# Optimization experiments

Measured on AMD Instinct MI355X. Metric: run time of the kernel, lower is better.

## Reference

```python
import jax, jax.numpy as jnp
import numpy as np
from jax import lax

T = 5        # unrolled ISTA iterations (module default)
LAM = 0.1    # soft-threshold level (module default)
B, L, K = 4096, 4096, 128


def _conv1d_same(x, k):
    """TF-style SAME cross-correlation. x: [B, L], k: [K] -> [B, L]."""
    Kw = k.shape[0]
    pad_left = (Kw - 1) // 2
    pad_right = Kw - 1 - pad_left
    out = lax.conv_general_dilated(
        x[:, None, :],            # [B, 1, L]
        k[None, None, :],         # [O=1, I=1, K]
        window_strides=(1,),
        padding=[(pad_left, pad_right)],
        dimension_numbers=("NCH", "OIH", "NCH"),
    )
    return out[:, 0, :]


def setup_inputs() -> dict:
    key = jax.random.key(0)
    k1, k2 = jax.random.split(key)
    y = jax.random.normal(k1, (B, L), dtype=jnp.float32)
    thz_pulse = jax.random.normal(k2, (K,), dtype=jnp.float32)  # learned pulse (trainable)
    step_size = jnp.full((1,), 0.1, dtype=jnp.float32)          # learned step (trainable)
    return {"y": y, "thz_pulse": thz_pulse, "step_size": step_size}


def reference(y, thz_pulse, step_size):
    x = jnp.zeros_like(y)
    h = thz_pulse           # matched-filter kernel
    h_rev = thz_pulse[::-1] # time-reversed kernel (adjoint / correlation)
    s = step_size[0]
    for _ in range(T):
        conv_out = _conv1d_same(y, h)           # H y
        residual = y - conv_out                 # y - H y
        update = _conv1d_same(residual, h_rev)  # H^T residual
        x = x + s * update                      # gradient step
        x = jnp.sign(x) * jax.nn.relu(jnp.abs(x) - LAM)  # soft-threshold
    return x
```

## Files before the change

### kernel.cpp

```cpp
#include <hip/hip_runtime.h>


typedef __bf16 bf16;
typedef __bf16 bf16x4 __attribute__((ext_vector_type(4)));
typedef __bf16 bf16x8 __attribute__((ext_vector_type(8)));
typedef float f32x4 __attribute__((ext_vector_type(4)));

#define LC 512
#define PY 824
#define LAM 0.1f
#define WS_AG 0
#define WS_A1 8192
#define WS_A2 12288
#define PYE 360
#define PRE 216

__global__ __launch_bounds__(256) void ista_prep(const float* __restrict__ h,
                                                 bf16* __restrict__ ws) {
  __shared__ float hs[256];
  __shared__ float acp[256];
  __shared__ bf16 gp[384];
  const int tid = threadIdx.x;
  hs[tid] = (tid < 128) ? h[tid] : 0.f;
  gp[tid] = (bf16)0.f;
  if (tid < 128) gp[256 + tid] = (bf16)0.f;
  __syncthreads();
  const int tau = tid & 127;
  {
    const int m0 = (tid >> 7) * 64;
    float p0 = 0.f, p1 = 0.f, p2 = 0.f, p3 = 0.f;
    for (int m = m0; m < m0 + 64; m += 4) {
      p0 += hs[m] * hs[m + tau];     p1 += hs[m + 1] * hs[m + 1 + tau];
      p2 += hs[m + 2] * hs[m + 2 + tau]; p3 += hs[m + 3] * hs[m + 3 + tau];
    }
    acp[tid] = (p0 + p1) + (p2 + p3);
  }
  __syncthreads();
  if (tid < 128) {
    float ac = acp[tid] + acp[tid + 128];
    float g1 = (tau <= 63) ? hs[63 - tau] : 0.f;
    gp[145 + tau] = (bf16)(g1 - ac);
    if (tau > 0) {
      float g2 = (tau <= 64) ? hs[63 + tau] : 0.f;
      gp[145 - tau] = (bf16)(g2 - ac);
    }
  }
  __syncthreads();
  for (int i = tid; i < 1024; i += 256) {
    const int l = i >> 4, dd = i & 15;
    if (dd < 9) {
      const int o = 144 + (l >> 4) * 8 - (l & 15) + (dd - 4) * 32;
      bf16x8 a;
#pragma unroll
      for (int j = 0; j < 8; ++j) a[j] = gp[o + j];
      *reinterpret_cast<bf16x8*>(ws + WS_AG + l * 128 + dd * 8) = a;
    }
  }
  for (int i = tid; i < 512; i += 256) {
    const int l = i >> 3, dd = i & 7;
    if (dd < 5) {
      const int o = 127 + (l >> 4) * 8 - (l & 15) + (dd - 2) * 32;
      bf16x8 a1, a2;
#pragma unroll
      for (int j = 0; j < 8; ++j) {
        int p = o + j;
        int i1 = p - 64;
        a1[j] = ((unsigned)i1 < 128u) ? (bf16)hs[i1] : (bf16)0.f;
        int i2 = 191 - p;
        a2[j] = ((unsigned)i2 < 128u) ? (bf16)(-hs[i2]) : (bf16)0.f;
      }
      *reinterpret_cast<bf16x8*>(ws + WS_A1 + l * 64 + dd * 8) = a1;
      *reinterpret_cast<bf16x8*>(ws + WS_A2 + l * 64 + dd * 8) = a2;
    }
  }
}

__global__ __launch_bounds__(256) void ista_fused(
    const float* __restrict__ y, const bf16* __restrict__ ws,
    const float* __restrict__ step, float* __restrict__ out) {
  __shared__ __align__(16) bf16 buf[16 * PY];
  const int tid = threadIdx.x;
  const int lane = tid & 63;
  const int li = lane & 15;
  const int quad = lane >> 4;
  const int wave = tid >> 6;
  const int bid = blockIdx.x;
  const float s = step[0];

  if (bid < 2048) {
    const int chunk0 = (bid >> 8) * LC;
    const int b0 = (bid & 255) * 16;

    bf16x8 AG[9];
#pragma unroll
    for (int dd = 0; dd < 9; ++dd)
      AG[dd] = *reinterpret_cast<const bf16x8*>(ws + WS_AG + lane * 128 + dd * 8);

    {
      const int rr = tid >> 4;
      const int t = tid & 15;
      const float* yrow = y + (size_t)(b0 + rr) * 4096;
      bf16* dst = buf + rr * PY;
      if (chunk0 != 0 && chunk0 != 3584) {
#pragma unroll
        for (int k = 0; k < 13; ++k) {
          int s4 = t + 16 * k;
          if (s4 < 200) {
            float4 v = *reinterpret_cast<const float4*>(yrow + chunk0 - 128 + s4 * 4);
            bf16x4 bv;
            bv[0] = (bf16)v.x; bv[1] = (bf16)v.y; bv[2] = (bf16)v.z; bv[3] = (bf16)v.w;
            *reinterpret_cast<bf16x4*>(dst + s4 * 4) = bv;
          }
        }
      } else {
#pragma unroll
        for (int k = 0; k < 13; ++k) {
          int s4 = t + 16 * k;
          if (s4 < 200) {
            int l = chunk0 - 128 + s4 * 4;
            float4 v;
            if (l >= 0 && l <= 4096 - 4) {
              v = *reinterpret_cast<const float4*>(yrow + l);
            } else {
              v.x = ((unsigned)(l + 0) < 4096u) ? yrow[l + 0] : 0.f;
              v.y = ((unsigned)(l + 1) < 4096u) ? yrow[l + 1] : 0.f;
              v.z = ((unsigned)(l + 2) < 4096u) ? yrow[l + 2] : 0.f;
              v.w = ((unsigned)(l + 3) < 4096u) ? yrow[l + 3] : 0.f;
            }
            bf16x4 bv;
            bv[0] = (bf16)v.x; bv[1] = (bf16)v.y; bv[2] = (bf16)v.z; bv[3] = (bf16)v.w;
            *reinterpret_cast<bf16x4*>(dst + s4 * 4) = bv;
          }
        }
      }
    }
    __syncthreads();

    const bf16* brow = buf + li * PY + 128 + quad * 8;
    const int iw = 16 * wave;
    bf16x8 B[9];
#pragma unroll
    for (int dd = 0; dd < 9; ++dd)
      B[dd] = *reinterpret_cast<const bf16x8*>(brow + iw + (dd - 4) * 32);
    float* orow = out + (size_t)(b0 + li) * 4096 + chunk0 + iw + quad * 4;
#pragma unroll
    for (int k = 0; k < 8; ++k) {
      f32x4 acc0 = {0.f, 0.f, 0.f, 0.f};
      f32x4 acc1 = {0.f, 0.f, 0.f, 0.f};
      acc0 = __builtin_amdgcn_mfma_f32_16x16x32_bf16(AG[0], B[0], acc0, 0, 0, 0);
      acc1 = __builtin_amdgcn_mfma_f32_16x16x32_bf16(AG[1], B[1], acc1, 0, 0, 0);
      acc0 = __builtin_amdgcn_mfma_f32_16x16x32_bf16(AG[2], B[2], acc0, 0, 0, 0);
      acc1 = __builtin_amdgcn_mfma_f32_16x16x32_bf16(AG[3], B[3], acc1, 0, 0, 0);
      acc0 = __builtin_amdgcn_mfma_f32_16x16x32_bf16(AG[4], B[4], acc0, 0, 0, 0);
      acc1 = __builtin_amdgcn_mfma_f32_16x16x32_bf16(AG[5], B[5], acc1, 0, 0, 0);
      acc0 = __builtin_amdgcn_mfma_f32_16x16x32_bf16(AG[6], B[6], acc0, 0, 0, 0);
      acc1 = __builtin_amdgcn_mfma_f32_16x16x32_bf16(AG[7], B[7], acc1, 0, 0, 0);
      acc0 = __builtin_amdgcn_mfma_f32_16x16x32_bf16(AG[8], B[8], acc0, 0, 0, 0);
      const int gc0 = chunk0 + iw + 64 * k;
      if (gc0 >= 64 && gc0 < 4032) {
        float4 xv;
#pragma unroll
        for (int e = 0; e < 4; ++e) {
          float su = s * (acc0[e] + acc1[e]);
          float ax = fabsf(su) - LAM;
          ax = ax > 0.f ? ax : 0.f;
          (&xv.x)[e] = 5.f * copysignf(ax, su);
        }
        *reinterpret_cast<float4*>(orow + 64 * k) = xv;
      }
      if (k < 7) {
#pragma unroll
        for (int r = 0; r < 7; ++r) B[r] = B[r + 2];
        B[7] = *reinterpret_cast<const bf16x8*>(brow + iw + 64 * (k + 1) + 96);
        B[8] = *reinterpret_cast<const bf16x8*>(brow + iw + 64 * (k + 1) + 128);
      }
    }
  } else {
    const int eid = bid - 2048;
    const int chunk0 = (eid & 1) ? (4096 - 64) : 0;
    const int b0 = (eid >> 1) * 16;
    bf16* ys = buf;
    bf16* rs = buf + 16 * PYE;

    bf16x8 A1[5], A2[5];
#pragma unroll
    for (int dd = 0; dd < 5; ++dd) {
      A1[dd] = *reinterpret_cast<const bf16x8*>(ws + WS_A1 + lane * 64 + dd * 8);
      A2[dd] = *reinterpret_cast<const bf16x8*>(ws + WS_A2 + lane * 64 + dd * 8);
    }

    {
      const int rr = tid >> 4;
      const int t = tid & 15;
      const float* yrow = y + (size_t)(b0 + rr) * 4096;
      bf16* dst = ys + rr * PYE;
#pragma unroll
      for (int k = 0; k < 6; ++k) {
        int s4 = t + 16 * k;
        if (s4 < 88) {
          int l = chunk0 - 128 + s4 * 4;
          float4 v;
          if (l >= 0 && l <= 4096 - 4) {
            v = *reinterpret_cast<const float4*>(yrow + l);
          } else {
            v.x = ((unsigned)(l + 0) < 4096u) ? yrow[l + 0] : 0.f;
            v.y = ((unsigned)(l + 1) < 4096u) ? yrow[l + 1] : 0.f;
            v.z = ((unsigned)(l + 2) < 4096u) ? yrow[l + 2] : 0.f;
            v.w = ((unsigned)(l + 3) < 4096u) ? yrow[l + 3] : 0.f;
          }
          bf16x4 bv;
          bv[0] = (bf16)v.x; bv[1] = (bf16)v.y; bv[2] = (bf16)v.z; bv[3] = (bf16)v.w;
          *reinterpret_cast<bf16x4*>(dst + s4 * 4) = bv;
        }
      }
    }
    __syncthreads();

    for (int t = wave; t < 13; t += 4) {
      const int i0 = -64 + 16 * t;
      f32x4 acc;
      {
        bf16x4 yv = *reinterpret_cast<const bf16x4*>(
            ys + li * PYE + (i0 + 128) + quad * 4);
        acc[0] = -(float)yv[0]; acc[1] = -(float)yv[1];
        acc[2] = -(float)yv[2]; acc[3] = -(float)yv[3];
      }
#pragma unroll
      for (int dd = 0; dd < 5; ++dd) {
        bf16x8 b = *reinterpret_cast<const bf16x8*>(
            ys + li * PYE + (i0 + (dd - 2) * 32 + 128) + quad * 8);
        acc = __builtin_amdgcn_mfma_f32_16x16x32_bf16(A1[dd], b, acc, 0, 0, 0);
      }
      bf16x4 rv;
#pragma unroll
      for (int e = 0; e < 4; ++e) {
        int g = chunk0 + i0 + quad * 4 + e;
        float v = ((unsigned)g < 4096u) ? acc[e] : 0.f;
        rv[e] = (bf16)v;
      }
      *reinterpret_cast<bf16x4*>(rs + li * PRE + (i0 + 64) + quad * 4) = rv;
    }
    __syncthreads();

    {
      const int i0 = 16 * wave;
      f32x4 acc = {0.f, 0.f, 0.f, 0.f};
#pragma unroll
      for (int dd = 0; dd < 5; ++dd) {
        bf16x8 b = *reinterpret_cast<const bf16x8*>(
            rs + li * PRE + (i0 + (dd - 2) * 32 + 64) + quad * 8);
        acc = __builtin_amdgcn_mfma_f32_16x16x32_bf16(A2[dd], b, acc, 0, 0, 0);
      }
      float4 xv;
#pragma unroll
      for (int e = 0; e < 4; ++e) {
        float su = s * acc[e];
        float ax = fabsf(su) - LAM;
        ax = ax > 0.f ? ax : 0.f;
        (&xv.x)[e] = 5.f * copysignf(ax, su);
      }
      *reinterpret_cast<float4*>(
          out + (size_t)(b0 + li) * 4096 + chunk0 + i0 + quad * 4) = xv;
    }
  }
}

extern "C" void kernel_launch(void* const* d_in, const int* in_sizes, int n_in,
                              void* d_out, int out_size, void* d_ws,
                              size_t ws_size, hipStream_t stream) {
  const float* y = (const float*)d_in[0];
  const float* h = (const float*)d_in[1];
  const float* s = (const float*)d_in[2];
  float* out = (float*)d_out;
  bf16* ws = (bf16*)d_ws;
  ista_prep<<<dim3(1), dim3(256), 0, stream>>>(h, ws);
  ista_fused<<<dim3(2048 + 512), dim3(256), 0, stream>>>(y, ws, s, out);
}
```

Measured before the change: 133.1 us.

## Load interior conv windows directly from global memory, dropping LDS staging

The interior path no longer stages a bf16 copy of the y tile in shared memory behind a block barrier. Each lane now loads its own 8-element windows straight from global memory, converts them to bf16 in registers, and prefetches the next two windows ahead of the MFMA chain. The shared buffer shrinks to what the edge path needs, and launch bounds now request 4 blocks per CU. The cost is redundant global loads, since neighbouring windows overlap and are fetched several times through the cache instead of once.

```diff
diff --git a/kernel.cpp b/kernel.cpp
--- a/kernel.cpp
+++ b/kernel.cpp
@@ -7,7 +7,6 @@
 typedef float f32x4 __attribute__((ext_vector_type(4)));
 
 #define LC 512
-#define PY 824
 #define LAM 0.1f
 #define WS_AG 0
 #define WS_A1 8192
@@ -75,10 +74,95 @@
   }
 }
 
-__global__ __launch_bounds__(256) void ista_fused(
+template <bool SAFE>
+__device__ __forceinline__ bf16x8 load_win(const float* __restrict__ yrow,
+                                           int c) {
+  bf16x8 b;
+  if (SAFE || (c >= 0 && c <= 4096 - 8)) {
+    float4 v0 = *reinterpret_cast<const float4*>(yrow + c);
+    float4 v1 = *reinterpret_cast<const float4*>(yrow + c + 4);
+    b[0] = (bf16)v0.x; b[1] = (bf16)v0.y; b[2] = (bf16)v0.z; b[3] = (bf16)v0.w;
+    b[4] = (bf16)v1.x; b[5] = (bf16)v1.y; b[6] = (bf16)v1.z; b[7] = (bf16)v1.w;
+  } else {
+#pragma unroll
+    for (int j = 0; j < 8; ++j) {
+      int cc = c + j;
+      b[j] = ((unsigned)cc < 4096u) ? (bf16)yrow[cc] : (bf16)0.f;
+    }
+  }
+  return b;
+}
+
+template <bool SAFE>
+__device__ __forceinline__ void interior_path(
+    const float* __restrict__ y, const bf16* __restrict__ ws, float s,
+    float* __restrict__ out, int chunk0, int b0, int lane) {
+  const int li = lane & 15;
+  const int quad = lane >> 4;
+  const int wave = (threadIdx.x) >> 6;
+
+  bf16x8 AG[9];
+#pragma unroll
+  for (int dd = 0; dd < 9; ++dd)
+    AG[dd] = *reinterpret_cast<const bf16x8*>(ws + WS_AG + lane * 128 + dd * 8);
+
+  const float* yrow = y + (size_t)(b0 + li) * 4096;
+  const int iw = 16 * wave;
+  const int cb = chunk0 + iw + quad * 8;
+
+  bf16x8 B[9];
+#pragma unroll
+  for (int dd = 0; dd < 9; ++dd)
+    B[dd] = load_win<SAFE>(yrow, cb + (dd - 4) * 32);
+
+  float* orow = out + (size_t)(b0 + li) * 4096 + chunk0 + iw + quad * 4;
+#pragma unroll
+  for (int k = 0; k < 8; ++k) {
+    bf16x8 n0, n1;
+    if (k < 7) {
+      n0 = load_win<SAFE>(yrow, cb + 64 * (k + 1) + 96);
+      n1 = load_win<SAFE>(yrow, cb + 64 * (k + 1) + 128);
+    }
+    f32x4 acc0 = {0.f, 0.f, 0.f, 0.f};
+    f32x4 acc1 = {0.f, 0.f, 0.f, 0.f};
+    acc0 = __builtin_amdgcn_mfma_f32_16x16x32_bf16(AG[0], B[0], acc0, 0, 0, 0);
+    acc1 = __builtin_amdgcn_mfma_f32_16x16x32_bf16(AG[1], B[1], acc1, 0, 0, 0);
+    acc0 = __builtin_amdgcn_mfma_f32_16x16x32_bf16(AG[2], B[2], acc0, 0, 0, 0);
+    acc1 = __builtin_amdgcn_mfma_f32_16x16x32_bf16(AG[3], B[3], acc1, 0, 0, 0);
+    acc0 = __builtin_amdgcn_mfma_f32_16x16x32_bf16(AG[4], B[4], acc0, 0, 0, 0);
+    acc1 = __builtin_amdgcn_mfma_f32_16x16x32_bf16(AG[5], B[5], acc1, 0, 0, 0);
+    acc0 = __builtin_amdgcn_mfma_f32_16x16x32_bf16(AG[6], B[6], acc0, 0, 0, 0);
+    acc1 = __builtin_amdgcn_mfma_f32_16x16x32_bf16(AG[7], B[7], acc1, 0, 0, 0);
+    acc0 = __builtin_amdgcn_mfma_f32_16x16x32_bf16(AG[8], B[8], acc0, 0, 0, 0);
+    bool do_store = true;
+    if (!SAFE) {
+      const int gc0 = chunk0 + iw + 64 * k;
+      do_store = (gc0 >= 64 && gc0 < 4032);
+    }
+    if (do_store) {
+      float4 xv;
+#pragma unroll
+      for (int e = 0; e < 4; ++e) {
+        float su = s * (acc0[e] + acc1[e]);
+        float ax = fabsf(su) - LAM;
+        ax = ax > 0.f ? ax : 0.f;
+        (&xv.x)[e] = 5.f * copysignf(ax, su);
+      }
+      *reinterpret_cast<float4*>(orow + 64 * k) = xv;
+    }
+    if (k < 7) {
+#pragma unroll
+      for (int r = 0; r < 7; ++r) B[r] = B[r + 2];
+      B[7] = n0;
+      B[8] = n1;
+    }
+  }
+}
+
+__global__ __launch_bounds__(256, 4) void ista_fused(
     const float* __restrict__ y, const bf16* __restrict__ ws,
     const float* __restrict__ step, float* __restrict__ out) {
-  __shared__ __align__(16) bf16 buf[16 * PY];
+  __shared__ __align__(16) bf16 buf[16 * PYE + 16 * PRE];
   const int tid = threadIdx.x;
   const int lane = tid & 63;
   const int li = lane & 15;
@@ -90,90 +174,10 @@
   if (bid < 2048) {
     const int chunk0 = (bid >> 8) * LC;
     const int b0 = (bid & 255) * 16;
-
-    bf16x8 AG[9];
-#pragma unroll
-    for (int dd = 0; dd < 9; ++dd)
-      AG[dd] = *reinterpret_cast<const bf16x8*>(ws + WS_AG + lane * 128 + dd * 8);
-
-    {
-      const int rr = tid >> 4;
-      const int t = tid & 15;
-      const float* yrow = y + (size_t)(b0 + rr) * 4096;
-      bf16* dst = buf + rr * PY;
-      if (chunk0 != 0 && chunk0 != 3584) {
-#pragma unroll
-        for (int k = 0; k < 13; ++k) {
-          int s4 = t + 16 * k;
-          if (s4 < 200) {
-            float4 v = *reinterpret_cast<const float4*>(yrow + chunk0 - 128 + s4 * 4);
-            bf16x4 bv;
-            bv[0] = (bf16)v.x; bv[1] = (bf16)v.y; bv[2] = (bf16)v.z; bv[3] = (bf16)v.w;
-            *reinterpret_cast<bf16x4*>(dst + s4 * 4) = bv;
-          }
-        }
-      } else {
-#pragma unroll
-        for (int k = 0; k < 13; ++k) {
-          int s4 = t + 16 * k;
-          if (s4 < 200) {
-            int l = chunk0 - 128 + s4 * 4;
-            float4 v;
-            if (l >= 0 && l <= 4096 - 4) {
-              v = *reinterpret_cast<const float4*>(yrow + l);
-            } else {
-              v.x = ((unsigned)(l + 0) < 4096u) ? yrow[l + 0] : 0.f;
-              v.y = ((unsigned)(l + 1) < 4096u) ? yrow[l + 1] : 0.f;
-              v.z = ((unsigned)(l + 2) < 4096u) ? yrow[l + 2] : 0.f;
-              v.w = ((unsigned)(l + 3) < 4096u) ? yrow[l + 3] : 0.f;
-            }
-            bf16x4 bv;
-            bv[0] = (bf16)v.x; bv[1] = (bf16)v.y; bv[2] = (bf16)v.z; bv[3] = (bf16)v.w;
-            *reinterpret_cast<bf16x4*>(dst + s4 * 4) = bv;
-          }
-        }
-      }
-    }
-    __syncthreads();
-
-    const bf16* brow = buf + li * PY + 128 + quad * 8;
-    const int iw = 16 * wave;
-    bf16x8 B[9];
-#pragma unroll
-    for (int dd = 0; dd < 9; ++dd)
-      B[dd] = *reinterpret_cast<const bf16x8*>(brow + iw + (dd - 4) * 32);
-    float* orow = out + (size_t)(b0 + li) * 4096 + chunk0 + iw + quad * 4;
-#pragma unroll
-    for (int k = 0; k < 8; ++k) {
-      f32x4 acc0 = {0.f, 0.f, 0.f, 0.f};
-      f32x4 acc1 = {0.f, 0.f, 0.f, 0.f};
-      acc0 = __builtin_amdgcn_mfma_f32_16x16x32_bf16(AG[0], B[0], acc0, 0, 0, 0);
-      acc1 = __builtin_amdgcn_mfma_f32_16x16x32_bf16(AG[1], B[1], acc1, 0, 0, 0);
-      acc0 = __builtin_amdgcn_mfma_f32_16x16x32_bf16(AG[2], B[2], acc0, 0, 0, 0);
-      acc1 = __builtin_amdgcn_mfma_f32_16x16x32_bf16(AG[3], B[3], acc1, 0, 0, 0);
-      acc0 = __builtin_amdgcn_mfma_f32_16x16x32_bf16(AG[4], B[4], acc0, 0, 0, 0);
-      acc1 = __builtin_amdgcn_mfma_f32_16x16x32_bf16(AG[5], B[5], acc1, 0, 0, 0);
-      acc0 = __builtin_amdgcn_mfma_f32_16x16x32_bf16(AG[6], B[6], acc0, 0, 0, 0);
-      acc1 = __builtin_amdgcn_mfma_f32_16x16x32_bf16(AG[7], B[7], acc1, 0, 0, 0);
-      acc0 = __builtin_amdgcn_mfma_f32_16x16x32_bf16(AG[8], B[8], acc0, 0, 0, 0);
-      const int gc0 = chunk0 + iw + 64 * k;
-      if (gc0 >= 64 && gc0 < 4032) {
-        float4 xv;
-#pragma unroll
-        for (int e = 0; e < 4; ++e) {
-          float su = s * (acc0[e] + acc1[e]);
-          float ax = fabsf(su) - LAM;
-          ax = ax > 0.f ? ax : 0.f;
-          (&xv.x)[e] = 5.f * copysignf(ax, su);
-        }
-        *reinterpret_cast<float4*>(orow + 64 * k) = xv;
-      }
-      if (k < 7) {
-#pragma unroll
-        for (int r = 0; r < 7; ++r) B[r] = B[r + 2];
-        B[7] = *reinterpret_cast<const bf16x8*>(brow + iw + 64 * (k + 1) + 96);
-        B[8] = *reinterpret_cast<const bf16x8*>(brow + iw + 64 * (k + 1) + 128);
-      }
+    if (chunk0 != 0 && chunk0 != 3584) {
+      interior_path<true>(y, ws, s, out, chunk0, b0, lane);
+    } else {
+      interior_path<false>(y, ws, s, out, chunk0, b0, lane);
     }
   } else {
     const int eid = bid - 2048;
```

After: 167.1 us. +25.5%, slower.
